# Kernel tuning notes

Measured on AMD Instinct MI355X. Metric: run time of the kernel, lower is better.

## Reference

```python
import jax, jax.numpy as jnp
import numpy as np

B, C, N, H = 4, 256, 2048, 8
D = C // H
EPS = 1e-5

def setup_inputs() -> dict:
    key = jax.random.key(0)
    ks = jax.random.split(key, 5)
    return {
        "x": jax.random.normal(ks[0], (B, C, N), jnp.float32),
        "w_qkv": jax.random.normal(ks[1], (3 * C, C), jnp.float32) * (C ** -0.5),
        "b_qkv": jax.random.normal(ks[2], (3 * C,), jnp.float32) * 0.02,
        "w_proj": jax.random.normal(ks[3], (C, C), jnp.float32) * (C ** -0.5),
        "b_proj": jax.random.normal(ks[4], (C,), jnp.float32) * 0.02,
        "ln_g": jnp.ones((C,), jnp.float32),
        "ln_b": jnp.zeros((C,), jnp.float32),
    }

def reference(x, w_qkv, b_qkv, w_proj, b_proj, ln_g, ln_b):
    # QKV 1x1 conv == per-point linear: [B,3C,N]
    qkv = jnp.einsum('oc,bcn->bon', w_qkv, x) + b_qkv[:, None]
    # [B,3,H,D,N] -> q,k,v each [B,H,N,D]
    qkv = qkv.reshape(B, 3, H, D, N).transpose(1, 0, 2, 4, 3)
    q, k, v = qkv[0], qkv[1], qkv[2]
    scale = D ** -0.5
    attn = jax.nn.softmax(jnp.einsum('bhnd,bhmd->bhnm', q, k) * scale, axis=-1)
    # dropout is identity in eval mode
    out = jnp.einsum('bhnm,bhmd->bhnd', attn, v)  # [B,H,N,D]
    out = out.transpose(0, 1, 3, 2).reshape(B, C, N)
    out = jnp.einsum('oc,bcn->bon', w_proj, out) + b_proj[:, None]
    out = out + x
    # LayerNorm over channel dim
    o = out.transpose(0, 2, 1)  # [B,N,C]
    mu = jnp.mean(o, axis=-1, keepdims=True)
    var = jnp.mean((o - mu) ** 2, axis=-1, keepdims=True)
    o = (o - mu) * jax.lax.rsqrt(var + EPS) * ln_g + ln_b
    return o.transpose(0, 2, 1)  # [B,C,N]
```

## Files before the change

kernel.cpp:

```cpp
#include <hip/hip_runtime.h>
#include <hip/hip_bf16.h>

#define Bx 4
#define Cx 256
#define Nx 2048
#define Hx 8
#define Dx 32

typedef __attribute__((ext_vector_type(8))) short bf16x8;
typedef __attribute__((ext_vector_type(4))) float f32x4;

#define QSCALE 0.25503494f

static __device__ __forceinline__ unsigned short f2bf(float f) {
    unsigned int u = __float_as_uint(f);
    u += 0x7fffu + ((u >> 16) & 1u);
    return (unsigned short)(u >> 16);
}
static __device__ __forceinline__ float bf2f(unsigned short u) {
    return __uint_as_float(((unsigned int)u) << 16);
}

__global__ __launch_bounds__(256) void convert_kernel(
    const float* __restrict__ x, const float* __restrict__ w_qkv,
    const float* __restrict__ w_proj,
    unsigned short* __restrict__ Xt, unsigned short* __restrict__ Wqkvb,
    unsigned short* __restrict__ Wpb)
{
    const int bx = blockIdx.x, t = threadIdx.x;
    if (bx < 256) {
        const int nb = (bx & 31) * 256 + t;
        const int b = nb >> 11, n = nb & 2047;
        const int c0 = (bx >> 5) * 32;
        const float* xb = x + ((size_t)b * Cx) * Nx + n;
        unsigned short* dst = Xt + ((size_t)b * Nx + n) * Cx;
        #pragma unroll
        for (int c8 = 0; c8 < 32; c8 += 8) {
            float f[8];
            #pragma unroll
            for (int j = 0; j < 8; ++j) f[j] = xb[(size_t)(c0 + c8 + j) * Nx];
            uint4 pk;
            pk.x = (unsigned)f2bf(f[0]) | ((unsigned)f2bf(f[1]) << 16);
            pk.y = (unsigned)f2bf(f[2]) | ((unsigned)f2bf(f[3]) << 16);
            pk.z = (unsigned)f2bf(f[4]) | ((unsigned)f2bf(f[5]) << 16);
            pk.w = (unsigned)f2bf(f[6]) | ((unsigned)f2bf(f[7]) << 16);
            *(uint4*)&dst[c0 + c8] = pk;
        }
    } else {
        const int base = (bx - 256) * 65536;
        #pragma unroll 4
        for (int j = 0; j < 64; ++j) {
            const int flat = base + j * 1024 + t * 4;
            if (flat < 768 * 256) {
                const float sc = (flat < 256 * 256) ? QSCALE : 1.0f;
                const float4 f = *(const float4*)&w_qkv[flat];
                ushort4 o;
                o.x = f2bf(f.x * sc); o.y = f2bf(f.y * sc);
                o.z = f2bf(f.z * sc); o.w = f2bf(f.w * sc);
                *(ushort4*)&Wqkvb[flat] = o;
            } else {
                const int f2 = flat - 768 * 256;
                const float4 f = *(const float4*)&w_proj[f2];
                ushort4 o;
                o.x = f2bf(f.x); o.y = f2bf(f.y);
                o.z = f2bf(f.z); o.w = f2bf(f.w);
                *(ushort4*)&Wpb[f2] = o;
            }
        }
    }
}

__global__ __launch_bounds__(256) void qkv_kernel(
    const unsigned short* __restrict__ Wb, const unsigned short* __restrict__ Xt,
    const float* __restrict__ bias,
    unsigned short* __restrict__ Qb, unsigned short* __restrict__ Kb,
    unsigned short* __restrict__ Vb)
{
    const int t = threadIdx.x;
    const int wv = t >> 6, l = t & 63;
    const int g = l >> 4, c = l & 15;
    const int o0 = blockIdx.x * 128 + (wv >> 1) * 64;
    const int n0 = blockIdx.y * 128 + (wv & 1) * 64;
    const int b  = blockIdx.z;
    const int region = blockIdx.x >> 1;

    const unsigned short* XtB = Xt + ((size_t)b * Nx) * Cx;

    f32x4 acc[4][4];
    #pragma unroll
    for (int i = 0; i < 4; ++i)
        #pragma unroll
        for (int j = 0; j < 4; ++j) acc[i][j] = (f32x4){0.f, 0.f, 0.f, 0.f};

    for (int cc = 0; cc < Cx; cc += 32) {
        bf16x8 wf[4], xf[4];
        #pragma unroll
        for (int ti = 0; ti < 4; ++ti)
            wf[ti] = *(const bf16x8*)&Wb[(size_t)(o0 + ti * 16 + c) * Cx + cc + g * 8];
        #pragma unroll
        for (int tj = 0; tj < 4; ++tj)
            xf[tj] = *(const bf16x8*)&XtB[(size_t)(n0 + tj * 16 + c) * Cx + cc + g * 8];
        if (region < 2) {
            #pragma unroll
            for (int ti = 0; ti < 4; ++ti)
                #pragma unroll
                for (int tj = 0; tj < 4; ++tj)
                    acc[ti][tj] = __builtin_amdgcn_mfma_f32_16x16x32_bf16(
                        wf[ti], xf[tj], acc[ti][tj], 0, 0, 0);
        } else {
            #pragma unroll
            for (int ti = 0; ti < 4; ++ti)
                #pragma unroll
                for (int tj = 0; tj < 4; ++tj)
                    acc[ti][tj] = __builtin_amdgcn_mfma_f32_16x16x32_bf16(
                        xf[ti], wf[tj], acc[ti][tj], 0, 0, 0);
        }
    }

    if (region < 2) {
        unsigned short* dst = (region == 0) ? Qb : Kb;
        #pragma unroll
        for (int ti = 0; ti < 4; ++ti) {
            const int o = o0 + ti * 16 + g * 4;
            float4 bv = *(const float4*)&bias[o];
            if (region == 0) { bv.x *= QSCALE; bv.y *= QSCALE; bv.z *= QSCALE; bv.w *= QSCALE; }
            const int d0 = o & 31, bh = b * 8 + ((o >> 5) & 7);
            unsigned short* dp = dst + ((size_t)bh * Nx) * Dx + d0;
            #pragma unroll
            for (int tj = 0; tj < 4; ++tj) {
                const int n = n0 + tj * 16 + c;
                ushort4 w4;
                w4.x = f2bf(acc[ti][tj][0] + bv.x);
                w4.y = f2bf(acc[ti][tj][1] + bv.y);
                w4.z = f2bf(acc[ti][tj][2] + bv.z);
                w4.w = f2bf(acc[ti][tj][3] + bv.w);
                *(ushort4*)&dp[(size_t)n * Dx] = w4;
            }
        }
    } else {
        #pragma unroll
        for (int tj = 0; tj < 4; ++tj) {
            const int o = o0 + tj * 16 + c;
            const float bv = bias[o];
            const int oV = o - 512, d = oV & 31, bh = b * 8 + (oV >> 5);
            unsigned short* dp = Vb + ((size_t)bh * Dx + d) * Nx;
            #pragma unroll
            for (int ti = 0; ti < 4; ++ti) {
                const int n = n0 + ti * 16 + g * 4;
                ushort4 w4;
                w4.x = f2bf(acc[ti][tj][0] + bv);
                w4.y = f2bf(acc[ti][tj][1] + bv);
                w4.z = f2bf(acc[ti][tj][2] + bv);
                w4.w = f2bf(acc[ti][tj][3] + bv);
                *(ushort4*)&dp[n] = w4;
            }
        }
    }
}

__global__ __launch_bounds__(256, 4) void attn_kernel(
    const unsigned short* __restrict__ Qb, const unsigned short* __restrict__ Kb,
    const unsigned short* __restrict__ Vb, unsigned short* __restrict__ Opart,
    float2* __restrict__ ML)
{
    const int t  = threadIdx.x;
    const int wv = t >> 6, l = t & 63;
    const int g  = l >> 4, c = l & 15;
    const int q0 = blockIdx.x * 128 + wv * 32;
    const int bh = blockIdx.y;
    const int z  = blockIdx.z;

    const unsigned short* Qp = Qb + (size_t)bh * Nx * Dx;
    const unsigned short* Kp = Kb + (size_t)bh * Nx * Dx;
    const unsigned short* Vp = Vb + (size_t)bh * Dx * Nx;

    bf16x8 qf[2];
    #pragma unroll
    for (int qt = 0; qt < 2; ++qt)
        qf[qt] = *(const bf16x8*)&Qp[(size_t)(q0 + qt * 16 + c) * Dx + g * 8];

    f32x4 oacc[2][2];
    #pragma unroll
    for (int i = 0; i < 2; ++i)
        #pragma unroll
        for (int j = 0; j < 2; ++j)
            oacc[i][j] = (f32x4){0.f, 0.f, 0.f, 0.f};
    float m_i[2] = {-3.0e38f, -3.0e38f};
    float l_i[2] = {0.f, 0.f};
    const f32x4 zacc = (f32x4){0.f, 0.f, 0.f, 0.f};

    const int rowperm = (c >> 2) * 8 + (c & 3);

    const int kv_beg = z * (Nx / 2), kv_end = kv_beg + (Nx / 2);
    for (int kv0 = kv_beg; kv0 < kv_end; kv0 += 64) {
        bf16x8 kf[4];
        kf[0] = *(const bf16x8*)&Kp[(size_t)(kv0 + rowperm +  0) * Dx + g * 8];
        kf[1] = *(const bf16x8*)&Kp[(size_t)(kv0 + rowperm +  4) * Dx + g * 8];
        kf[2] = *(const bf16x8*)&Kp[(size_t)(kv0 + rowperm + 32) * Dx + g * 8];
        kf[3] = *(const bf16x8*)&Kp[(size_t)(kv0 + rowperm + 36) * Dx + g * 8];
        bf16x8 vf[2][2];
        #pragma unroll
        for (int dt = 0; dt < 2; ++dt)
            #pragma unroll
            for (int kc = 0; kc < 2; ++kc)
                vf[dt][kc] = *(const bf16x8*)
                    &Vp[(size_t)(dt * 16 + c) * Nx + kv0 + kc * 32 + g * 8];

        #pragma unroll
        for (int qt = 0; qt < 2; ++qt) {
            f32x4 sacc[4];
            #pragma unroll
            for (int ct = 0; ct < 4; ++ct)
                sacc[ct] = __builtin_amdgcn_mfma_f32_16x16x32_bf16(
                    kf[ct], qf[qt], zacc, 0, 0, 0);

            float mx = -3.0e38f;
            #pragma unroll
            for (int ct = 0; ct < 4; ++ct)
                #pragma unroll
                for (int r = 0; r < 4; ++r) mx = fmaxf(mx, sacc[ct][r]);
            mx = fmaxf(mx, __shfl_xor(mx, 16, 64));
            mx = fmaxf(mx, __shfl_xor(mx, 32, 64));
            if (mx > m_i[qt] + 8.f) {
                const float aq = exp2f(m_i[qt] - mx);
                m_i[qt] = mx;
                l_i[qt] *= aq;
                #pragma unroll
                for (int dt = 0; dt < 2; ++dt)
                    #pragma unroll
                    for (int r = 0; r < 4; ++r) oacc[dt][qt][r] *= aq;
            }
            const float mcur = m_i[qt];
            float rs = 0.f;
            unsigned int pw[4][2];
            #pragma unroll
            for (int ct = 0; ct < 4; ++ct) {
                float p[4];
                #pragma unroll
                for (int r = 0; r < 4; ++r) {
                    p[r] = exp2f(sacc[ct][r] - mcur);
                    rs += p[r];
                }
                pw[ct][0] = (__float_as_uint(p[0]) >> 16) |
                            (__float_as_uint(p[1]) & 0xffff0000u);
                pw[ct][1] = (__float_as_uint(p[2]) >> 16) |
                            (__float_as_uint(p[3]) & 0xffff0000u);
            }
            rs += __shfl_xor(rs, 16, 64);
            rs += __shfl_xor(rs, 32, 64);
            l_i[qt] += rs;

            #pragma unroll
            for (int kc = 0; kc < 2; ++kc) {
                union { unsigned int u[4]; bf16x8 v; } bw;
                bw.u[0] = pw[kc * 2 + 0][0];
                bw.u[1] = pw[kc * 2 + 0][1];
                bw.u[2] = pw[kc * 2 + 1][0];
                bw.u[3] = pw[kc * 2 + 1][1];
                oacc[0][qt] = __builtin_amdgcn_mfma_f32_16x16x32_bf16(
                    vf[0][kc], bw.v, oacc[0][qt], 0, 0, 0);
                oacc[1][qt] = __builtin_amdgcn_mfma_f32_16x16x32_bf16(
                    vf[1][kc], bw.v, oacc[1][qt], 0, 0, 0);
            }
        }
    }

    unsigned short* Op = Opart + ((size_t)(z * 32 + bh)) * Nx * Dx;
    float2* Mlp = ML + (size_t)(z * 32 + bh) * Nx;
    #pragma unroll
    for (int qt = 0; qt < 2; ++qt) {
        const int q = q0 + qt * 16 + c;
        if (g == 0) Mlp[q] = make_float2(m_i[qt], l_i[qt]);
        #pragma unroll
        for (int dt = 0; dt < 2; ++dt) {
            ushort4 w4;
            w4.x = f2bf(oacc[dt][qt][0]);
            w4.y = f2bf(oacc[dt][qt][1]);
            w4.z = f2bf(oacc[dt][qt][2]);
            w4.w = f2bf(oacc[dt][qt][3]);
            *(ushort4*)&Op[(size_t)q * Dx + dt * 16 + g * 4] = w4;
        }
    }
}

__global__ __launch_bounds__(256) void merge_kernel(
    const unsigned short* __restrict__ Opart, const float2* __restrict__ ML,
    unsigned short* __restrict__ Abf)
{
    const int i = blockIdx.x * 256 + threadIdx.x;
    const int qg = i >> 3;
    const int d0 = (i & 7) * 4;
    const int bh = qg >> 11, q = qg & 2047;
    const int b = bh >> 3, h = bh & 7;

    const float2 e0 = ML[qg];
    const float2 e1 = ML[65536 + qg];
    const float M  = fmaxf(e0.x, e1.x);
    const float a0 = exp2f(e0.x - M), a1 = exp2f(e1.x - M);
    const float inv = 1.f / (e0.y * a0 + e1.y * a1);
    const float w0 = a0 * inv, w1 = a1 * inv;

    const size_t base = (size_t)qg * Dx + d0;
    const ushort4 p0 = *(const ushort4*)&Opart[base];
    const ushort4 p1 = *(const ushort4*)&Opart[(size_t)65536 * Dx + base];
    ushort4 o;
    o.x = f2bf(bf2f(p0.x) * w0 + bf2f(p1.x) * w1);
    o.y = f2bf(bf2f(p0.y) * w0 + bf2f(p1.y) * w1);
    o.z = f2bf(bf2f(p0.z) * w0 + bf2f(p1.z) * w1);
    o.w = f2bf(bf2f(p0.w) * w0 + bf2f(p1.w) * w1);
    *(ushort4*)&Abf[((size_t)b * Nx + q) * Cx + h * 32 + d0] = o;
}

__global__ __launch_bounds__(256) void proj_ln_kernel(
    const unsigned short* __restrict__ Abf, const unsigned short* __restrict__ Wpb,
    const float* __restrict__ bp, const float* __restrict__ x,
    const float* __restrict__ lng, const float* __restrict__ lnb,
    float* __restrict__ out)
{
    __shared__ float red[4][32];
    __shared__ float redq[4][32];
    __shared__ float mv[2][32];

    const int t  = threadIdx.x;
    const int wv = t >> 6, l = t & 63;
    const int lg = l >> 4, lc = l & 15;
    const int n0 = blockIdx.x * 32;
    const int b  = blockIdx.y;
    const int o0 = wv * 64;

    const unsigned short* Ab = Abf + ((size_t)b * Nx) * Cx;

    f32x4 acc[4][2];
    #pragma unroll
    for (int i = 0; i < 4; ++i)
        #pragma unroll
        for (int j = 0; j < 2; ++j) acc[i][j] = (f32x4){0.f, 0.f, 0.f, 0.f};

    for (int cc = 0; cc < Cx; cc += 32) {
        bf16x8 wf[4], af[2];
        #pragma unroll
        for (int ti = 0; ti < 4; ++ti)
            wf[ti] = *(const bf16x8*)&Wpb[(size_t)(o0 + ti * 16 + lc) * Cx + cc + lg * 8];
        #pragma unroll
        for (int tj = 0; tj < 2; ++tj)
            af[tj] = *(const bf16x8*)&Ab[(size_t)(n0 + tj * 16 + lc) * Cx + cc + lg * 8];
        #pragma unroll
        for (int ti = 0; ti < 4; ++ti)
            #pragma unroll
            for (int tj = 0; tj < 2; ++tj)
                acc[ti][tj] = __builtin_amdgcn_mfma_f32_16x16x32_bf16(
                    wf[ti], af[tj], acc[ti][tj], 0, 0, 0);
    }

    #pragma unroll
    for (int ti = 0; ti < 4; ++ti) {
        const int o = o0 + ti * 16 + lg * 4;
        const float4 bv = *(const float4*)&bp[o];
        #pragma unroll
        for (int tj = 0; tj < 2; ++tj) {
            const int n = n0 + tj * 16 + lc;
            const float* xp = &x[((size_t)b * Cx + o) * Nx + n];
            acc[ti][tj][0] += bv.x + xp[0];
            acc[ti][tj][1] += bv.y + xp[Nx];
            acc[ti][tj][2] += bv.z + xp[2 * Nx];
            acc[ti][tj][3] += bv.w + xp[3 * Nx];
        }
    }

    float s[2] = {0.f, 0.f}, q[2] = {0.f, 0.f};
    #pragma unroll
    for (int ti = 0; ti < 4; ++ti)
        #pragma unroll
        for (int tj = 0; tj < 2; ++tj)
            #pragma unroll
            for (int r = 0; r < 4; ++r) {
                const float v = acc[ti][tj][r];
                s[tj] += v; q[tj] += v * v;
            }
    #pragma unroll
    for (int tj = 0; tj < 2; ++tj) {
        s[tj] += __shfl_xor(s[tj], 16, 64);
        s[tj] += __shfl_xor(s[tj], 32, 64);
        q[tj] += __shfl_xor(q[tj], 16, 64);
        q[tj] += __shfl_xor(q[tj], 32, 64);
    }
    if (lg == 0) {
        #pragma unroll
        for (int tj = 0; tj < 2; ++tj) {
            red[wv][tj * 16 + lc]  = s[tj];
            redq[wv][tj * 16 + lc] = q[tj];
        }
    }
    __syncthreads();
    if (t < 32) {
        const float S = red[0][t] + red[1][t] + red[2][t] + red[3][t];
        const float Q = redq[0][t] + redq[1][t] + redq[2][t] + redq[3][t];
        const float mu  = S * (1.f / 256.f);
        const float var = Q * (1.f / 256.f) - mu * mu;
        mv[0][t] = mu;
        mv[1][t] = rsqrtf(var + 1e-5f);
    }
    __syncthreads();

    float mu_[2], rs_[2];
    #pragma unroll
    for (int tj = 0; tj < 2; ++tj) {
        mu_[tj] = mv[0][tj * 16 + lc];
        rs_[tj] = mv[1][tj * 16 + lc];
    }
    #pragma unroll
    for (int ti = 0; ti < 4; ++ti) {
        const int o = o0 + ti * 16 + lg * 4;
        const float4 g4 = *(const float4*)&lng[o];
        const float4 b4 = *(const float4*)&lnb[o];
        const float gr[4] = {g4.x, g4.y, g4.z, g4.w};
        const float br[4] = {b4.x, b4.y, b4.z, b4.w};
        #pragma unroll
        for (int tj = 0; tj < 2; ++tj) {
            const int n = n0 + tj * 16 + lc;
            float* op = &out[((size_t)b * Cx + o) * Nx + n];
            #pragma unroll
            for (int r = 0; r < 4; ++r)
                op[(size_t)r * Nx] =
                    (acc[ti][tj][r] - mu_[tj]) * rs_[tj] * gr[r] + br[r];
        }
    }
}

extern "C" void kernel_launch(void* const* d_in, const int* in_sizes, int n_in,
                              void* d_out, int out_size, void* d_ws, size_t ws_size,
                              hipStream_t stream) {
    (void)in_sizes; (void)n_in; (void)out_size; (void)ws_size;
    const float* x      = (const float*)d_in[0];
    const float* w_qkv  = (const float*)d_in[1];
    const float* b_qkv  = (const float*)d_in[2];
    const float* w_proj = (const float*)d_in[3];
    const float* b_proj = (const float*)d_in[4];
    const float* ln_g   = (const float*)d_in[5];
    const float* ln_b   = (const float*)d_in[6];
    float* out = (float*)d_out;

    char* wsb = (char*)d_ws;
    unsigned short* Xt    = (unsigned short*)(wsb);
    unsigned short* Wqkvb = (unsigned short*)(wsb + (size_t)4 * 1024 * 1024);
    unsigned short* Wpb   = (unsigned short*)(wsb + (size_t)4 * 1024 * 1024 + 393216);
    unsigned short* Qb    = (unsigned short*)(wsb + (size_t)5 * 1024 * 1024);
    unsigned short* Kb    = (unsigned short*)(wsb + (size_t)9 * 1024 * 1024);
    unsigned short* Vb    = (unsigned short*)(wsb + (size_t)13 * 1024 * 1024);
    unsigned short* Abf   = (unsigned short*)(wsb + (size_t)17 * 1024 * 1024);
    unsigned short* Opart = (unsigned short*)(wsb + (size_t)21 * 1024 * 1024);
    float2*         ML    = (float2*)(wsb + (size_t)29 * 1024 * 1024);

    convert_kernel<<<dim3(260), 256, 0, stream>>>(x, w_qkv, w_proj, Xt, Wqkvb, Wpb);
    qkv_kernel<<<dim3(6, 16, 4), 256, 0, stream>>>(Wqkvb, Xt, b_qkv, Qb, Kb, Vb);
    attn_kernel<<<dim3(16, 32, 2), 256, 0, stream>>>(Qb, Kb, Vb, Opart, ML);
    merge_kernel<<<dim3(2048), 256, 0, stream>>>(Opart, ML, Abf);
    proj_ln_kernel<<<dim3(64, 4), 256, 0, stream>>>(Abf, Wpb, b_proj, x,
                                                    ln_g, ln_b, out);
}
```

Baseline: 180.0 us.

## Fuse split-KV merge into projection, remap blocks across XCDs, shrink tiles

Removes the separate merge kernel: proj_ln now rescales and combines the two partial attention outputs with their max/sum stats while loading its GEMM operand, so the Abf round trip and one launch disappear. qkv and attn blocks are renumbered so neighbouring work lands on the same XCD, which should improve L2 locality. The convert, qkv and proj grids get smaller per-block tiles and more blocks to raise occupancy. The cost is recomputing merge weights per output tile and less reuse per block.

```diff
diff --git a/kernel.cpp b/kernel.cpp
--- a/kernel.cpp
+++ b/kernel.cpp
@@ -28,14 +28,14 @@
     unsigned short* __restrict__ Wpb)
 {
     const int bx = blockIdx.x, t = threadIdx.x;
-    if (bx < 256) {
+    if (bx < 512) {
         const int nb = (bx & 31) * 256 + t;
         const int b = nb >> 11, n = nb & 2047;
-        const int c0 = (bx >> 5) * 32;
-        const float* xb = x + ((size_t)b * Cx) * Nx + n;
+        const int c0 = (bx >> 5) * 16;
+        const float* xb = x + (size_t)b * Cx * Nx + n;
         unsigned short* dst = Xt + ((size_t)b * Nx + n) * Cx;
         #pragma unroll
-        for (int c8 = 0; c8 < 32; c8 += 8) {
+        for (int c8 = 0; c8 < 16; c8 += 8) {
             float f[8];
             #pragma unroll
             for (int j = 0; j < 8; ++j) f[j] = xb[(size_t)(c0 + c8 + j) * Nx];
@@ -47,24 +47,24 @@
             *(uint4*)&dst[c0 + c8] = pk;
         }
     } else {
-        const int base = (bx - 256) * 65536;
-        #pragma unroll 4
-        for (int j = 0; j < 64; ++j) {
-            const int flat = base + j * 1024 + t * 4;
-            if (flat < 768 * 256) {
-                const float sc = (flat < 256 * 256) ? QSCALE : 1.0f;
-                const float4 f = *(const float4*)&w_qkv[flat];
+        const int flat = (bx - 512) * 2048 + t * 8;
+        #pragma unroll
+        for (int hh = 0; hh < 8; hh += 4) {
+            const int f0 = flat + hh;
+            if (f0 < 768 * 256) {
+                const float sc = (f0 < 65536) ? QSCALE : 1.0f;
+                const float4 f = *(const float4*)&w_qkv[f0];
                 ushort4 o;
                 o.x = f2bf(f.x * sc); o.y = f2bf(f.y * sc);
                 o.z = f2bf(f.z * sc); o.w = f2bf(f.w * sc);
-                *(ushort4*)&Wqkvb[flat] = o;
+                *(ushort4*)&Wqkvb[f0] = o;
             } else {
-                const int f2 = flat - 768 * 256;
-                const float4 f = *(const float4*)&w_proj[f2];
+                const int f2v = f0 - 768 * 256;
+                const float4 f = *(const float4*)&w_proj[f2v];
                 ushort4 o;
                 o.x = f2bf(f.x); o.y = f2bf(f.y);
                 o.z = f2bf(f.z); o.w = f2bf(f.w);
-                *(ushort4*)&Wpb[f2] = o;
+                *(ushort4*)&Wpb[f2v] = o;
             }
         }
     }
@@ -79,53 +79,50 @@
     const int t = threadIdx.x;
     const int wv = t >> 6, l = t & 63;
     const int g = l >> 4, c = l & 15;
-    const int o0 = blockIdx.x * 128 + (wv >> 1) * 64;
-    const int n0 = blockIdx.y * 128 + (wv & 1) * 64;
-    const int b  = blockIdx.z;
-    const int region = blockIdx.x >> 1;
-
-    const unsigned short* XtB = Xt + ((size_t)b * Nx) * Cx;
-
-    f32x4 acc[4][4];
-    #pragma unroll
-    for (int i = 0; i < 4; ++i)
-        #pragma unroll
-        for (int j = 0; j < 4; ++j) acc[i][j] = (f32x4){0.f, 0.f, 0.f, 0.f};
-
-    for (int cc = 0; cc < Cx; cc += 32) {
-        bf16x8 wf[4], xf[4];
-        #pragma unroll
-        for (int ti = 0; ti < 4; ++ti)
-            wf[ti] = *(const bf16x8*)&Wb[(size_t)(o0 + ti * 16 + c) * Cx + cc + g * 8];
-        #pragma unroll
-        for (int tj = 0; tj < 4; ++tj)
-            xf[tj] = *(const bf16x8*)&XtB[(size_t)(n0 + tj * 16 + c) * Cx + cc + g * 8];
-        if (region < 2) {
-            #pragma unroll
-            for (int ti = 0; ti < 4; ++ti)
+
+    const int lin = blockIdx.x + 12 * (blockIdx.y + 16 * blockIdx.z);
+    const int xcd = lin & 7, s = lin >> 3;
+    const int xb = s % 12;
+    const int yz = (s / 12) * 8 + xcd;
+    const int yb = yz & 15, b = yz >> 4;
+
+    const int o0 = xb * 64 + (wv >> 1) * 32;
+    const int n0 = yb * 128 + (wv & 1) * 64;
+    const int region = xb >> 2;
+
+    const unsigned short* XtB = Xt + (size_t)b * Nx * Cx;
+
+    if (region < 2) {
+        f32x4 acc[2][4];
+        #pragma unroll
+        for (int i = 0; i < 2; ++i)
+            #pragma unroll
+            for (int j = 0; j < 4; ++j) acc[i][j] = (f32x4){0.f, 0.f, 0.f, 0.f};
+
+        for (int cc = 0; cc < Cx; cc += 32) {
+            bf16x8 wf[2], xf[4];
+            #pragma unroll
+            for (int ti = 0; ti < 2; ++ti)
+                wf[ti] = *(const bf16x8*)&Wb[(size_t)(o0 + ti * 16 + c) * Cx + cc + g * 8];
+            #pragma unroll
+            for (int tj = 0; tj < 4; ++tj)
+                xf[tj] = *(const bf16x8*)&XtB[(size_t)(n0 + tj * 16 + c) * Cx + cc + g * 8];
+            #pragma unroll
+            for (int ti = 0; ti < 2; ++ti)
                 #pragma unroll
                 for (int tj = 0; tj < 4; ++tj)
                     acc[ti][tj] = __builtin_amdgcn_mfma_f32_16x16x32_bf16(
                         wf[ti], xf[tj], acc[ti][tj], 0, 0, 0);
-        } else {
-            #pragma unroll
-            for (int ti = 0; ti < 4; ++ti)
-                #pragma unroll
-                for (int tj = 0; tj < 4; ++tj)
-                    acc[ti][tj] = __builtin_amdgcn_mfma_f32_16x16x32_bf16(
-                        xf[ti], wf[tj], acc[ti][tj], 0, 0, 0);
-        }
-    }
-
-    if (region < 2) {
+        }
+
         unsigned short* dst = (region == 0) ? Qb : Kb;
         #pragma unroll
-        for (int ti = 0; ti < 4; ++ti) {
+        for (int ti = 0; ti < 2; ++ti) {
             const int o = o0 + ti * 16 + g * 4;
             float4 bv = *(const float4*)&bias[o];
             if (region == 0) { bv.x *= QSCALE; bv.y *= QSCALE; bv.z *= QSCALE; bv.w *= QSCALE; }
             const int d0 = o & 31, bh = b * 8 + ((o >> 5) & 7);
-            unsigned short* dp = dst + ((size_t)bh * Nx) * Dx + d0;
+            unsigned short* dp = dst + (size_t)bh * Nx * Dx + d0;
             #pragma unroll
             for (int tj = 0; tj < 4; ++tj) {
                 const int n = n0 + tj * 16 + c;
@@ -138,20 +135,42 @@
             }
         }
     } else {
-        #pragma unroll
-        for (int tj = 0; tj < 4; ++tj) {
-            const int o = o0 + tj * 16 + c;
+        f32x4 acc[4][2];
+        #pragma unroll
+        for (int i = 0; i < 4; ++i)
+            #pragma unroll
+            for (int j = 0; j < 2; ++j) acc[i][j] = (f32x4){0.f, 0.f, 0.f, 0.f};
+
+        for (int cc = 0; cc < Cx; cc += 32) {
+            bf16x8 wf[2], xf[4];
+            #pragma unroll
+            for (int ot = 0; ot < 2; ++ot)
+                wf[ot] = *(const bf16x8*)&Wb[(size_t)(o0 + ot * 16 + c) * Cx + cc + g * 8];
+            #pragma unroll
+            for (int nt = 0; nt < 4; ++nt)
+                xf[nt] = *(const bf16x8*)&XtB[(size_t)(n0 + nt * 16 + c) * Cx + cc + g * 8];
+            #pragma unroll
+            for (int nt = 0; nt < 4; ++nt)
+                #pragma unroll
+                for (int ot = 0; ot < 2; ++ot)
+                    acc[nt][ot] = __builtin_amdgcn_mfma_f32_16x16x32_bf16(
+                        xf[nt], wf[ot], acc[nt][ot], 0, 0, 0);
+        }
+
+        #pragma unroll
+        for (int ot = 0; ot < 2; ++ot) {
+            const int o = o0 + ot * 16 + c;
             const float bv = bias[o];
             const int oV = o - 512, d = oV & 31, bh = b * 8 + (oV >> 5);
             unsigned short* dp = Vb + ((size_t)bh * Dx + d) * Nx;
             #pragma unroll
-            for (int ti = 0; ti < 4; ++ti) {
-                const int n = n0 + ti * 16 + g * 4;
+            for (int nt = 0; nt < 4; ++nt) {
+                const int n = n0 + nt * 16 + g * 4;
                 ushort4 w4;
-                w4.x = f2bf(acc[ti][tj][0] + bv);
-                w4.y = f2bf(acc[ti][tj][1] + bv);
-                w4.z = f2bf(acc[ti][tj][2] + bv);
-                w4.w = f2bf(acc[ti][tj][3] + bv);
+                w4.x = f2bf(acc[nt][ot][0] + bv);
+                w4.y = f2bf(acc[nt][ot][1] + bv);
+                w4.z = f2bf(acc[nt][ot][2] + bv);
+                w4.w = f2bf(acc[nt][ot][3] + bv);
                 *(ushort4*)&dp[n] = w4;
             }
         }
@@ -166,9 +185,13 @@
     const int t  = threadIdx.x;
     const int wv = t >> 6, l = t & 63;
     const int g  = l >> 4, c = l & 15;
-    const int q0 = blockIdx.x * 128 + wv * 32;
-    const int bh = blockIdx.y;
-    const int z  = blockIdx.z;
+
+    const int lin = blockIdx.x + 16 * blockIdx.y + 512 * blockIdx.z;
+    const int xcd = lin & 7, s = lin >> 3;
+    const int bh = ((s & 3) << 3) | xcd;
+    const int qt_ = (s >> 2) & 15;
+    const int z  = s >> 6;
+    const int q0 = qt_ * 128 + wv * 32;
 
     const unsigned short* Qp = Qb + (size_t)bh * Nx * Dx;
     const unsigned short* Kp = Kb + (size_t)bh * Nx * Dx;
@@ -283,116 +306,86 @@
     }
 }
 
-__global__ __launch_bounds__(256) void merge_kernel(
+__global__ __launch_bounds__(256) void proj_ln_kernel(
     const unsigned short* __restrict__ Opart, const float2* __restrict__ ML,
-    unsigned short* __restrict__ Abf)
-{
-    const int i = blockIdx.x * 256 + threadIdx.x;
-    const int qg = i >> 3;
-    const int d0 = (i & 7) * 4;
-    const int bh = qg >> 11, q = qg & 2047;
-    const int b = bh >> 3, h = bh & 7;
-
-    const float2 e0 = ML[qg];
-    const float2 e1 = ML[65536 + qg];
-    const float M  = fmaxf(e0.x, e1.x);
-    const float a0 = exp2f(e0.x - M), a1 = exp2f(e1.x - M);
-    const float inv = 1.f / (e0.y * a0 + e1.y * a1);
-    const float w0 = a0 * inv, w1 = a1 * inv;
-
-    const size_t base = (size_t)qg * Dx + d0;
-    const ushort4 p0 = *(const ushort4*)&Opart[base];
-    const ushort4 p1 = *(const ushort4*)&Opart[(size_t)65536 * Dx + base];
-    ushort4 o;
-    o.x = f2bf(bf2f(p0.x) * w0 + bf2f(p1.x) * w1);
-    o.y = f2bf(bf2f(p0.y) * w0 + bf2f(p1.y) * w1);
-    o.z = f2bf(bf2f(p0.z) * w0 + bf2f(p1.z) * w1);
-    o.w = f2bf(bf2f(p0.w) * w0 + bf2f(p1.w) * w1);
-    *(ushort4*)&Abf[((size_t)b * Nx + q) * Cx + h * 32 + d0] = o;
-}
-
-__global__ __launch_bounds__(256) void proj_ln_kernel(
-    const unsigned short* __restrict__ Abf, const unsigned short* __restrict__ Wpb,
+    const unsigned short* __restrict__ Wpb,
     const float* __restrict__ bp, const float* __restrict__ x,
     const float* __restrict__ lng, const float* __restrict__ lnb,
     float* __restrict__ out)
 {
-    __shared__ float red[4][32];
-    __shared__ float redq[4][32];
-    __shared__ float mv[2][32];
+    __shared__ float red[4][16];
+    __shared__ float redq[4][16];
+    __shared__ float mv[2][16];
 
     const int t  = threadIdx.x;
     const int wv = t >> 6, l = t & 63;
     const int lg = l >> 4, lc = l & 15;
-    const int n0 = blockIdx.x * 32;
+    const int n0 = blockIdx.x * 16;
     const int b  = blockIdx.y;
     const int o0 = wv * 64;
-
-    const unsigned short* Ab = Abf + ((size_t)b * Nx) * Cx;
-
-    f32x4 acc[4][2];
-    #pragma unroll
-    for (int i = 0; i < 4; ++i)
-        #pragma unroll
-        for (int j = 0; j < 2; ++j) acc[i][j] = (f32x4){0.f, 0.f, 0.f, 0.f};
+    const int n  = n0 + lc;
+
+    f32x4 acc[4];
+    #pragma unroll
+    for (int i = 0; i < 4; ++i) acc[i] = (f32x4){0.f, 0.f, 0.f, 0.f};
 
     for (int cc = 0; cc < Cx; cc += 32) {
-        bf16x8 wf[4], af[2];
-        #pragma unroll
-        for (int ti = 0; ti < 4; ++ti)
-            wf[ti] = *(const bf16x8*)&Wpb[(size_t)(o0 + ti * 16 + lc) * Cx + cc + lg * 8];
-        #pragma unroll
-        for (int tj = 0; tj < 2; ++tj)
-            af[tj] = *(const bf16x8*)&Ab[(size_t)(n0 + tj * 16 + lc) * Cx + cc + lg * 8];
-        #pragma unroll
-        for (int ti = 0; ti < 4; ++ti)
-            #pragma unroll
-            for (int tj = 0; tj < 2; ++tj)
-                acc[ti][tj] = __builtin_amdgcn_mfma_f32_16x16x32_bf16(
-                    wf[ti], af[tj], acc[ti][tj], 0, 0, 0);
+        const int h = cc >> 5;
+        const int bh = b * 8 + h;
+        const float2 e0 = ML[(size_t)bh * Nx + n];
+        const float2 e1 = ML[(size_t)(32 + bh) * Nx + n];
+        const float M  = fmaxf(e0.x, e1.x);
+        const float a0 = exp2f(e0.x - M), a1 = exp2f(e1.x - M);
+        const float inv = 1.f / (e0.y * a0 + e1.y * a1);
+        const float w0 = a0 * inv, w1 = a1 * inv;
+        const size_t obase = ((size_t)bh * Nx + n) * Dx + lg * 8;
+        const uint4 u0 = *(const uint4*)&Opart[obase];
+        const uint4 u1 = *(const uint4*)&Opart[(size_t)65536 * Dx + obase];
+        const unsigned int u0w[4] = {u0.x, u0.y, u0.z, u0.w};
+        const unsigned int u1w[4] = {u1.x, u1.y, u1.z, u1.w};
+        union { unsigned int u[4]; bf16x8 v; } af;
+        #pragma unroll
+        for (int wi = 0; wi < 4; ++wi) {
+            const float lo = bf2f((unsigned short)(u0w[wi] & 0xffffu)) * w0 +
+                             bf2f((unsigned short)(u1w[wi] & 0xffffu)) * w1;
+            const float hi = bf2f((unsigned short)(u0w[wi] >> 16)) * w0 +
+                             bf2f((unsigned short)(u1w[wi] >> 16)) * w1;
+            af.u[wi] = (unsigned int)f2bf(lo) | ((unsigned int)f2bf(hi) << 16);
+        }
+        #pragma unroll
+        for (int ti = 0; ti < 4; ++ti) {
+            const bf16x8 wf = *(const bf16x8*)
+                &Wpb[(size_t)(o0 + ti * 16 + lc) * Cx + cc + lg * 8];
+            acc[ti] = __builtin_amdgcn_mfma_f32_16x16x32_bf16(wf, af.v, acc[ti], 0, 0, 0);
+        }
     }
 
     #pragma unroll
     for (int ti = 0; ti < 4; ++ti) {
         const int o = o0 + ti * 16 + lg * 4;
         const float4 bv = *(const float4*)&bp[o];
-        #pragma unroll
-        for (int tj = 0; tj < 2; ++tj) {
-            const int n = n0 + tj * 16 + lc;
-            const float* xp = &x[((size_t)b * Cx + o) * Nx + n];
-            acc[ti][tj][0] += bv.x + xp[0];
-            acc[ti][tj][1] += bv.y + xp[Nx];
-            acc[ti][tj][2] += bv.z + xp[2 * Nx];
-            acc[ti][tj][3] += bv.w + xp[3 * Nx];
-        }
-    }
-
-    float s[2] = {0.f, 0.f}, q[2] = {0.f, 0.f};
+        const float* xp = &x[((size_t)b * Cx + o) * Nx + n];
+        acc[ti][0] += bv.x + xp[0];
+        acc[ti][1] += bv.y + xp[Nx];
+        acc[ti][2] += bv.z + xp[2 * Nx];
+        acc[ti][3] += bv.w + xp[3 * Nx];
+    }
+
+    float s_ = 0.f, q_ = 0.f;
     #pragma unroll
     for (int ti = 0; ti < 4; ++ti)
         #pragma unroll
-        for (int tj = 0; tj < 2; ++tj)
-            #pragma unroll
-            for (int r = 0; r < 4; ++r) {
-                const float v = acc[ti][tj][r];
-                s[tj] += v; q[tj] += v * v;
-            }
-    #pragma unroll
-    for (int tj = 0; tj < 2; ++tj) {
-        s[tj] += __shfl_xor(s[tj], 16, 64);
-        s[tj] += __shfl_xor(s[tj], 32, 64);
-        q[tj] += __shfl_xor(q[tj], 16, 64);
-        q[tj] += __shfl_xor(q[tj], 32, 64);
-    }
-    if (lg == 0) {
-        #pragma unroll
-        for (int tj = 0; tj < 2; ++tj) {
-            red[wv][tj * 16 + lc]  = s[tj];
-            redq[wv][tj * 16 + lc] = q[tj];
-        }
-    }
+        for (int r = 0; r < 4; ++r) {
+            const float v = acc[ti][r];
+            s_ += v; q_ += v * v;
+        }
+    s_ += __shfl_xor(s_, 16, 64);
+    s_ += __shfl_xor(s_, 32, 64);
+    q_ += __shfl_xor(q_, 16, 64);
+    q_ += __shfl_xor(q_, 32, 64);
+    if (lg == 0) { red[wv][lc] = s_; redq[wv][lc] = q_; }
     __syncthreads();
-    if (t < 32) {
+    if (t < 16) {
         const float S = red[0][t] + red[1][t] + red[2][t] + red[3][t];
         const float Q = redq[0][t] + redq[1][t] + redq[2][t] + redq[3][t];
         const float mu  = S * (1.f / 256.f);
@@ -402,12 +395,7 @@
     }
     __syncthreads();
 
-    float mu_[2], rs_[2];
-    #pragma unroll
-    for (int tj = 0; tj < 2; ++tj) {
-        mu_[tj] = mv[0][tj * 16 + lc];
-        rs_[tj] = mv[1][tj * 16 + lc];
-    }
+    const float mu_ = mv[0][lc], rs_ = mv[1][lc];
     #pragma unroll
     for (int ti = 0; ti < 4; ++ti) {
         const int o = o0 + ti * 16 + lg * 4;
@@ -415,15 +403,10 @@
         const float4 b4 = *(const float4*)&lnb[o];
         const float gr[4] = {g4.x, g4.y, g4.z, g4.w};
         const float br[4] = {b4.x, b4.y, b4.z, b4.w};
-        #pragma unroll
-        for (int tj = 0; tj < 2; ++tj) {
-            const int n = n0 + tj * 16 + lc;
-            float* op = &out[((size_t)b * Cx + o) * Nx + n];
-            #pragma unroll
-            for (int r = 0; r < 4; ++r)
-                op[(size_t)r * Nx] =
-                    (acc[ti][tj][r] - mu_[tj]) * rs_[tj] * gr[r] + br[r];
-        }
+        float* op = &out[((size_t)b * Cx + o) * Nx + n];
+        #pragma unroll
+        for (int r = 0; r < 4; ++r)
+            op[(size_t)r * Nx] = (acc[ti][r] - mu_) * rs_ * gr[r] + br[r];
     }
 }
 
@@ -447,14 +430,12 @@
     unsigned short* Qb    = (unsigned short*)(wsb + (size_t)5 * 1024 * 1024);
     unsigned short* Kb    = (unsigned short*)(wsb + (size_t)9 * 1024 * 1024);
     unsigned short* Vb    = (unsigned short*)(wsb + (size_t)13 * 1024 * 1024);
-    unsigned short* Abf   = (unsigned short*)(wsb + (size_t)17 * 1024 * 1024);
     unsigned short* Opart = (unsigned short*)(wsb + (size_t)21 * 1024 * 1024);
     float2*         ML    = (float2*)(wsb + (size_t)29 * 1024 * 1024);
 
-    convert_kernel<<<dim3(260), 256, 0, stream>>>(x, w_qkv, w_proj, Xt, Wqkvb, Wpb);
-    qkv_kernel<<<dim3(6, 16, 4), 256, 0, stream>>>(Wqkvb, Xt, b_qkv, Qb, Kb, Vb);
+    convert_kernel<<<dim3(640), 256, 0, stream>>>(x, w_qkv, w_proj, Xt, Wqkvb, Wpb);
+    qkv_kernel<<<dim3(12, 16, 4), 256, 0, stream>>>(Wqkvb, Xt, b_qkv, Qb, Kb, Vb);
     attn_kernel<<<dim3(16, 32, 2), 256, 0, stream>>>(Qb, Kb, Vb, Opart, ML);
-    merge_kernel<<<dim3(2048), 256, 0, stream>>>(Opart, ML, Abf);
-    proj_ln_kernel<<<dim3(64, 4), 256, 0, stream>>>(Abf, Wpb, b_proj, x,
-                                                    ln_g, ln_b, out);
-}
+    proj_ln_kernel<<<dim3(128, 4), 256, 0, stream>>>(Opart, ML, Wpb, b_proj, x,
+                                                     ln_g, ln_b, out);
+}
```

Result: faster. 159.1 us (-11.6%).
